# Kernel optimization log

Hardware: AMD Instinct MI355X
Metric: run time of the kernel (lower is better)

## Reference

```python
import jax, jax.numpy as jnp
import numpy as np

H = 5          # num_heads
QHD = 32       # query/key head dim
PHD = 4        # pos head dim


def setup_inputs() -> dict:
    key = jax.random.key(0)
    ks = jax.random.split(key, 8)
    T, B, D, PD = 512, 64, 512, 192
    lm_pruned = jax.random.normal(ks[0], (T, B, D), jnp.float32)
    am_pruned = jax.random.normal(ks[1], (T, B, D), jnp.float32)
    pos_emb = jax.random.normal(ks[2], (1, 2 * T - 1, PD), jnp.float32)
    key_padding_mask = jnp.zeros((B, T), bool)
    scale_q = QHD ** (-0.25)
    W_lm = (jax.random.normal(ks[3], (D, (QHD + PHD) * H), jnp.float32) * (scale_q / np.sqrt(D))).astype(jnp.float32)
    b_lm = jnp.zeros(((QHD + PHD) * H,), jnp.float32)
    W_am = (jax.random.normal(ks[4], (D, QHD * H), jnp.float32) * (scale_q / np.sqrt(D))).astype(jnp.float32)
    b_am = jnp.zeros((QHD * H,), jnp.float32)
    W_pos = (jax.random.normal(ks[5], (PD, H * PHD), jnp.float32) * (0.05 / np.sqrt(PD))).astype(jnp.float32)
    return {"lm_pruned": lm_pruned, "am_pruned": am_pruned, "pos_emb": pos_emb,
            "key_padding_mask": key_padding_mask,
            "W_lm": W_lm, "b_lm": b_lm, "W_am": W_am, "b_am": b_am, "W_pos": W_pos}


def reference(lm_pruned, am_pruned, pos_emb, key_padding_mask, W_lm, b_lm, W_am, b_am, W_pos):
    T, B, _ = lm_pruned.shape
    S = am_pruned.shape[0]
    lm = lm_pruned @ W_lm + b_lm          # (T, B, (QHD+PHD)*H)
    am = am_pruned @ W_am + b_am          # (S, B, QHD*H)
    q = lm[..., : H * QHD].reshape(T, B, H, QHD)
    p = lm[..., H * QHD:].reshape(T, B, H, PHD)
    k = am.reshape(S, B, H, QHD)          # whiten/balance are value-identity
    # content scores: (H, B, T, S)
    attn_scores = jnp.einsum('tbhd,sbhd->hbts', q, k)
    # positional scores
    pe = (pos_emb[0] @ W_pos).reshape(2 * T - 1, H, PHD)   # (2T-1, H, PHD)
    pos_scores = jnp.einsum('tbhd,nhd->hbtn', p, pe)        # (H, B, T, 2T-1)
    # Transformer-XL rel-shift: out[..., i, j] = pos_scores[..., i, j - i + T - 1]
    idx = jnp.arange(T)[None, :] - jnp.arange(T)[:, None] + (T - 1)  # (T, T)
    shifted = jnp.take_along_axis(pos_scores, idx[None, None, :, :], axis=-1)  # (H,B,T,T)
    attn_scores = attn_scores + shifted
    # key padding mask: (B, S) -> broadcast over heads and query positions
    attn_scores = jnp.where(key_padding_mask[None, :, None, :], jnp.float32(-1000.0), attn_scores)
    return jax.nn.softmax(attn_scores, axis=-1)
```

## Files before the change

### kernel.cpp

```cpp
#include <hip/hip_runtime.h>

#define TT 512
#define BB 64
#define HH 5
#define DD 512
#define NPOS 1023

typedef __bf16 bf16x8 __attribute__((ext_vector_type(8)));
typedef float floatx4 __attribute__((ext_vector_type(4)));

__global__ void prep_w_kernel(const float* __restrict__ Wlm, const float* __restrict__ Wam,
                              __bf16* __restrict__ WlmT, __bf16* __restrict__ WamT) {
  int idx = blockIdx.x * 256 + threadIdx.x;
  if (idx < 192 * 512) {
    int n = idx >> 9, k = idx & 511;
    float v = (n < 180) ? Wlm[k * 180 + n] : 0.f;
    WlmT[idx] = (__bf16)v;
  }
  if (idx < 160 * 512) {
    int n = idx >> 9, k = idx & 511;
    WamT[idx] = (__bf16)Wam[k * 160 + n];
  }
}

__global__ void pe_proj_kernel(const float* __restrict__ pos_emb, const float* __restrict__ Wpos,
                               float* __restrict__ peT) {
  int n = blockIdx.x;
  __shared__ float row[192];
  for (int i = threadIdx.x; i < 192; i += 64) row[i] = pos_emb[n * 192 + i];
  __syncthreads();
  int c = threadIdx.x;
  if (c < 20) {
    float acc = 0.f;
    for (int pd = 0; pd < 192; ++pd) acc += row[pd] * Wpos[pd * 20 + c];
    int h = c >> 2, d = c & 3;
    peT[((size_t)h * NPOS + n) * 4 + d] = acc;
  }
}

template <int NT, bool IS_LM>
__global__ __launch_bounds__(256) void proj_kernel(
    const float* __restrict__ A, const __bf16* __restrict__ WT, const float* __restrict__ bias,
    __bf16* __restrict__ qk_out, float* __restrict__ p_out) {
  __shared__ __align__(16) __bf16 a_lds[64][32];
  __shared__ __align__(16) __bf16 w_lds[NT * 16][32];
  const int tid = threadIdx.x;
  const int m0 = blockIdx.x * 64;
  const int lane = tid & 63, w = tid >> 6;
  const int quad = lane >> 4, nl = lane & 15;

  floatx4 zero = {0.f, 0.f, 0.f, 0.f};
  floatx4 acc[NT];
#pragma unroll
  for (int j = 0; j < NT; ++j) acc[j] = zero;

  const int arow = tid >> 2, aseg = tid & 3;
  for (int k0 = 0; k0 < 512; k0 += 32) {
    const float* ap = A + (size_t)(m0 + arow) * 512 + k0 + aseg * 8;
    float4 av0 = *(const float4*)ap;
    float4 av1 = *(const float4*)(ap + 4);
    __bf16* ad = &a_lds[arow][aseg * 8];
    ad[0] = (__bf16)av0.x; ad[1] = (__bf16)av0.y; ad[2] = (__bf16)av0.z; ad[3] = (__bf16)av0.w;
    ad[4] = (__bf16)av1.x; ad[5] = (__bf16)av1.y; ad[6] = (__bf16)av1.z; ad[7] = (__bf16)av1.w;
    for (int task = tid; task < NT * 64; task += 256) {
      int n = task >> 2, seg = task & 3;
      *(bf16x8*)&w_lds[n][seg * 8] = *(const bf16x8*)(WT + (size_t)n * 512 + k0 + seg * 8);
    }
    __syncthreads();
    bf16x8 af = *(const bf16x8*)&a_lds[16 * w + nl][quad * 8];
#pragma unroll
    for (int jt = 0; jt < NT; ++jt) {
      bf16x8 bfr = *(const bf16x8*)&w_lds[jt * 16 + nl][quad * 8];
      acc[jt] = __builtin_amdgcn_mfma_f32_16x16x32_bf16(af, bfr, acc[jt], 0, 0, 0);
    }
    __syncthreads();
  }
#pragma unroll
  for (int jt = 0; jt < NT; ++jt) {
    int c = jt * 16 + nl;
#pragma unroll
    for (int r = 0; r < 4; ++r) {
      int m = m0 + 16 * w + quad * 4 + r;
      float bv;
      if (IS_LM) bv = (c < 180) ? bias[c] : 0.f;
      else bv = bias[c];
      float val = acc[jt][r] + bv;
      if (IS_LM) {
        if (c < 160) qk_out[(size_t)m * 160 + c] = (__bf16)val;
        else if (c < 180) p_out[(size_t)m * 20 + (c - 160)] = val;
      } else {
        qk_out[(size_t)m * 160 + c] = (__bf16)val;
      }
    }
  }
}

__global__ __launch_bounds__(256) void attn_kernel(
    const __bf16* __restrict__ q, const __bf16* __restrict__ k,
    const float* __restrict__ p, const float* __restrict__ peT,
    const unsigned char* __restrict__ mask, float* __restrict__ out) {
  __shared__ __align__(16) __bf16 k_lds[512][32];
  __shared__ __align__(16) __bf16 q_lds[64][32];
  __shared__ __align__(16) float p_lds[64][4];
  __shared__ __align__(16) float pe_lds[575 * 4];
  __shared__ float mask_lds[512];

  const int tid = threadIdx.x;
  const int t0 = blockIdx.x * 64;
  const int b = blockIdx.y;
  const int h = blockIdx.z;
  const int lane = tid & 63, w = tid >> 6;
  const int quad = lane >> 4, nl = lane & 15;

#pragma unroll
  for (int it = 0; it < 8; ++it) {
    int idx = tid + it * 256;
    int s = idx >> 2, c = idx & 3;
    *(bf16x8*)&k_lds[s][c * 8] =
        *(const bf16x8*)(k + ((size_t)(s * BB + b) * HH + h) * 32 + c * 8);
  }
  {
    int s = tid >> 2, c = tid & 3;
    *(bf16x8*)&q_lds[s][c * 8] =
        *(const bf16x8*)(q + ((size_t)((t0 + s) * BB + b) * HH + h) * 32 + c * 8);
  }
  if (tid < 64) {
    *(float4*)&p_lds[tid][0] =
        *(const float4*)(p + ((size_t)((t0 + tid) * BB + b) * HH + h) * 4);
  }
  {
    int u0 = 448 - t0;
    for (int i = tid; i < 575; i += 256)
      *(float4*)&pe_lds[i * 4] = *(const float4*)(peT + ((size_t)h * NPOS + u0 + i) * 4);
  }
  for (int i = tid; i < 512; i += 256)
    mask_lds[i] = mask[b * 512 + i] ? -1000.f : 0.f;
  __syncthreads();

  floatx4 zero = {0.f, 0.f, 0.f, 0.f};
  floatx4 acc[32];
  bf16x8 af = *(const bf16x8*)&q_lds[16 * w + nl][quad * 8];
#pragma unroll
  for (int jt = 0; jt < 32; ++jt) {
    bf16x8 bfr = *(const bf16x8*)&k_lds[jt * 16 + nl][quad * 8];
    acc[jt] = __builtin_amdgcn_mfma_f32_16x16x32_bf16(af, bfr, zero, 0, 0, 0);
  }

  float rmax[4], rinv[4];
#pragma unroll
  for (int r = 0; r < 4; ++r) {
    int tl = 16 * w + quad * 4 + r;
    floatx4 pv = *(const floatx4*)&p_lds[tl][0];
    float mx = -3.4e38f;
#pragma unroll
    for (int jt = 0; jt < 32; ++jt) {
      int s = jt * 16 + nl;
      floatx4 pe = *(const floatx4*)&pe_lds[(s - tl + 63) * 4];
      float v = acc[jt][r] + pv[0] * pe[0] + pv[1] * pe[1] + pv[2] * pe[2] + pv[3] * pe[3] +
                mask_lds[s];
      acc[jt][r] = v;
      mx = fmaxf(mx, v);
    }
#pragma unroll
    for (int d = 1; d < 16; d <<= 1) mx = fmaxf(mx, __shfl_xor(mx, d, 64));
    rmax[r] = mx;
  }
#pragma unroll
  for (int r = 0; r < 4; ++r) {
    float sum = 0.f;
#pragma unroll
    for (int jt = 0; jt < 32; ++jt) {
      float e = __expf(acc[jt][r] - rmax[r]);
      acc[jt][r] = e;
      sum += e;
    }
#pragma unroll
    for (int d = 1; d < 16; d <<= 1) sum += __shfl_xor(sum, d, 64);
    rinv[r] = 1.0f / sum;
  }
#pragma unroll
  for (int r = 0; r < 4; ++r) {
    int tl = 16 * w + quad * 4 + r;
    size_t base = (((size_t)h * BB + b) * TT + (t0 + tl)) * TT;
#pragma unroll
    for (int jt = 0; jt < 32; ++jt) out[base + jt * 16 + nl] = acc[jt][r] * rinv[r];
  }
}

extern "C" void kernel_launch(void* const* d_in, const int* in_sizes, int n_in,
                              void* d_out, int out_size, void* d_ws, size_t ws_size,
                              hipStream_t stream) {
  const float* lm = (const float*)d_in[0];
  const float* am = (const float*)d_in[1];
  const float* pos_emb = (const float*)d_in[2];
  const unsigned char* mask = (const unsigned char*)d_in[3];
  const float* Wlm = (const float*)d_in[4];
  const float* blm = (const float*)d_in[5];
  const float* Wam = (const float*)d_in[6];
  const float* bam = (const float*)d_in[7];
  const float* Wpos = (const float*)d_in[8];
  float* out = (float*)d_out;

  char* ws = (char*)d_ws;
  __bf16* qbuf = (__bf16*)ws;
  __bf16* kbuf = qbuf + (size_t)32768 * 160;
  float* pbuf = (float*)(kbuf + (size_t)32768 * 160);
  float* pebuf = pbuf + (size_t)32768 * 20;
  __bf16* WlmT = (__bf16*)(pebuf + (size_t)5 * NPOS * 4);
  __bf16* WamT = WlmT + (size_t)192 * 512;

  prep_w_kernel<<<384, 256, 0, stream>>>(Wlm, Wam, WlmT, WamT);
  pe_proj_kernel<<<NPOS, 64, 0, stream>>>(pos_emb, Wpos, pebuf);
  proj_kernel<12, true><<<512, 256, 0, stream>>>(lm, WlmT, blm, qbuf, pbuf);
  proj_kernel<10, false><<<512, 256, 0, stream>>>(am, WamT, bam, kbuf, nullptr);
  attn_kernel<<<dim3(8, BB, HH), 256, 0, stream>>>(qbuf, kbuf, pbuf, pebuf, mask, out);
}
```

Before: 545.6 us.

## Merge prep and projection launches, store pos-emb in bf16, fold mask into MFMA

Combines the weight-transpose and positional-projection kernels into one launch, and the two projection GEMMs into a single 1024-block launch, cutting launch count from five to three. In the attention kernel, the projected positional embedding is stored as bf16 and unpacked with bit shifts. The key mask is fed in as the MFMA accumulator input, and the positional-score loop is restructured to compute all four row maxima in one pass. It also adds occupancy hints, vectorises the LDS store of A, and lowers positional-term precision to bf16, which may slightly change numerics.

Result: faster. 511.3 us (-6.3%).

```diff
diff --git a/kernel.cpp b/kernel.cpp
--- a/kernel.cpp
+++ b/kernel.cpp
@@ -3,75 +3,75 @@
 #define TT 512
 #define BB 64
 #define HH 5
-#define DD 512
 #define NPOS 1023
 
 typedef __bf16 bf16x8 __attribute__((ext_vector_type(8)));
+typedef __bf16 bf16x4 __attribute__((ext_vector_type(4)));
 typedef float floatx4 __attribute__((ext_vector_type(4)));
 
-__global__ void prep_w_kernel(const float* __restrict__ Wlm, const float* __restrict__ Wam,
-                              __bf16* __restrict__ WlmT, __bf16* __restrict__ WamT) {
-  int idx = blockIdx.x * 256 + threadIdx.x;
-  if (idx < 192 * 512) {
-    int n = idx >> 9, k = idx & 511;
-    float v = (n < 180) ? Wlm[k * 180 + n] : 0.f;
-    WlmT[idx] = (__bf16)v;
-  }
-  if (idx < 160 * 512) {
-    int n = idx >> 9, k = idx & 511;
-    WamT[idx] = (__bf16)Wam[k * 160 + n];
-  }
-}
-
-__global__ void pe_proj_kernel(const float* __restrict__ pos_emb, const float* __restrict__ Wpos,
-                               float* __restrict__ peT) {
-  int n = blockIdx.x;
-  __shared__ float row[192];
-  for (int i = threadIdx.x; i < 192; i += 64) row[i] = pos_emb[n * 192 + i];
-  __syncthreads();
-  int c = threadIdx.x;
-  if (c < 20) {
-    float acc = 0.f;
-    for (int pd = 0; pd < 192; ++pd) acc += row[pd] * Wpos[pd * 20 + c];
-    int h = c >> 2, d = c & 3;
-    peT[((size_t)h * NPOS + n) * 4 + d] = acc;
+__global__ void prep_kernel(const float* __restrict__ Wlm, const float* __restrict__ Wam,
+                            const float* __restrict__ pos_emb, const float* __restrict__ Wpos,
+                            __bf16* __restrict__ WlmT, __bf16* __restrict__ WamT,
+                            __bf16* __restrict__ peB) {
+  int bx = blockIdx.x;
+  if (bx < 384) {
+    int idx = bx * 256 + threadIdx.x;
+    if (idx < 192 * 512) {
+      int n = idx >> 9, k = idx & 511;
+      float v = (n < 180) ? Wlm[k * 180 + n] : 0.f;
+      WlmT[idx] = (__bf16)v;
+    }
+    if (idx < 160 * 512) {
+      int n = idx >> 9, k = idx & 511;
+      WamT[idx] = (__bf16)Wam[k * 160 + n];
+    }
+  } else {
+    int t = (bx - 384) * 256 + threadIdx.x;
+    int n = t >> 5, c = t & 31;
+    if (n < NPOS && c < 20) {
+      float acc = 0.f;
+#pragma unroll 8
+      for (int pd = 0; pd < 192; ++pd) acc += pos_emb[n * 192 + pd] * Wpos[pd * 20 + c];
+      int h = c >> 2, d = c & 3;
+      peB[((size_t)h * NPOS + n) * 4 + d] = (__bf16)acc;
+    }
   }
 }
 
 template <int NT, bool IS_LM>
-__global__ __launch_bounds__(256) void proj_kernel(
-    const float* __restrict__ A, const __bf16* __restrict__ WT, const float* __restrict__ bias,
-    __bf16* __restrict__ qk_out, float* __restrict__ p_out) {
-  __shared__ __align__(16) __bf16 a_lds[64][32];
-  __shared__ __align__(16) __bf16 w_lds[NT * 16][32];
+__device__ __forceinline__ void proj_body(const float* __restrict__ A, const __bf16* __restrict__ WT,
+                                          const float* __restrict__ bias, __bf16* __restrict__ qk_out,
+                                          float* __restrict__ p_out, int blk,
+                                          __bf16 (*a_lds)[32], __bf16 (*w_lds)[32]) {
   const int tid = threadIdx.x;
-  const int m0 = blockIdx.x * 64;
+  const int m0 = blk * 64;
   const int lane = tid & 63, w = tid >> 6;
   const int quad = lane >> 4, nl = lane & 15;
 
-  floatx4 zero = {0.f, 0.f, 0.f, 0.f};
   floatx4 acc[NT];
 #pragma unroll
-  for (int j = 0; j < NT; ++j) acc[j] = zero;
+  for (int j = 0; j < NT; ++j) acc[j] = floatx4{0.f, 0.f, 0.f, 0.f};
 
   const int arow = tid >> 2, aseg = tid & 3;
   for (int k0 = 0; k0 < 512; k0 += 32) {
     const float* ap = A + (size_t)(m0 + arow) * 512 + k0 + aseg * 8;
     float4 av0 = *(const float4*)ap;
     float4 av1 = *(const float4*)(ap + 4);
-    __bf16* ad = &a_lds[arow][aseg * 8];
-    ad[0] = (__bf16)av0.x; ad[1] = (__bf16)av0.y; ad[2] = (__bf16)av0.z; ad[3] = (__bf16)av0.w;
-    ad[4] = (__bf16)av1.x; ad[5] = (__bf16)av1.y; ad[6] = (__bf16)av1.z; ad[7] = (__bf16)av1.w;
+    bf16x8 pk;
+    pk[0] = (__bf16)av0.x; pk[1] = (__bf16)av0.y; pk[2] = (__bf16)av0.z; pk[3] = (__bf16)av0.w;
+    pk[4] = (__bf16)av1.x; pk[5] = (__bf16)av1.y; pk[6] = (__bf16)av1.z; pk[7] = (__bf16)av1.w;
+    *(bf16x8*)&a_lds[arow][aseg * 8] = pk;
+#pragma unroll
     for (int task = tid; task < NT * 64; task += 256) {
       int n = task >> 2, seg = task & 3;
       *(bf16x8*)&w_lds[n][seg * 8] = *(const bf16x8*)(WT + (size_t)n * 512 + k0 + seg * 8);
     }
     __syncthreads();
-    bf16x8 af = *(const bf16x8*)&a_lds[16 * w + nl][quad * 8];
+    bf16x8 afr = *(const bf16x8*)&a_lds[16 * w + nl][quad * 8];
 #pragma unroll
     for (int jt = 0; jt < NT; ++jt) {
       bf16x8 bfr = *(const bf16x8*)&w_lds[jt * 16 + nl][quad * 8];
-      acc[jt] = __builtin_amdgcn_mfma_f32_16x16x32_bf16(af, bfr, acc[jt], 0, 0, 0);
+      acc[jt] = __builtin_amdgcn_mfma_f32_16x16x32_bf16(afr, bfr, acc[jt], 0, 0, 0);
     }
     __syncthreads();
   }
@@ -81,9 +81,7 @@
 #pragma unroll
     for (int r = 0; r < 4; ++r) {
       int m = m0 + 16 * w + quad * 4 + r;
-      float bv;
-      if (IS_LM) bv = (c < 180) ? bias[c] : 0.f;
-      else bv = bias[c];
+      float bv = IS_LM ? ((c < 180) ? bias[c] : 0.f) : bias[c];
       float val = acc[jt][r] + bv;
       if (IS_LM) {
         if (c < 160) qk_out[(size_t)m * 160 + c] = (__bf16)val;
@@ -95,14 +93,27 @@
   }
 }
 
-__global__ __launch_bounds__(256) void attn_kernel(
+__global__ __launch_bounds__(256, 4) void proj_kernel(
+    const float* __restrict__ lm, const __bf16* __restrict__ WlmT, const float* __restrict__ blm,
+    __bf16* __restrict__ qbuf, float* __restrict__ pbuf,
+    const float* __restrict__ am, const __bf16* __restrict__ WamT, const float* __restrict__ bam,
+    __bf16* __restrict__ kbuf) {
+  __shared__ __align__(16) __bf16 a_lds[64][32];
+  __shared__ __align__(16) __bf16 w_lds[192][32];
+  if (blockIdx.x < 512)
+    proj_body<12, true>(lm, WlmT, blm, qbuf, pbuf, blockIdx.x, a_lds, w_lds);
+  else
+    proj_body<10, false>(am, WamT, bam, kbuf, nullptr, blockIdx.x - 512, a_lds, w_lds);
+}
+
+__global__ __launch_bounds__(256, 2) void attn_kernel(
     const __bf16* __restrict__ q, const __bf16* __restrict__ k,
-    const float* __restrict__ p, const float* __restrict__ peT,
+    const float* __restrict__ p, const __bf16* __restrict__ peB,
     const unsigned char* __restrict__ mask, float* __restrict__ out) {
   __shared__ __align__(16) __bf16 k_lds[512][32];
   __shared__ __align__(16) __bf16 q_lds[64][32];
   __shared__ __align__(16) float p_lds[64][4];
-  __shared__ __align__(16) float pe_lds[575 * 4];
+  __shared__ __align__(16) __bf16 pe_lds[576 * 4];
   __shared__ float mask_lds[512];
 
   const int tid = threadIdx.x;
@@ -117,60 +128,73 @@
     int idx = tid + it * 256;
     int s = idx >> 2, c = idx & 3;
     *(bf16x8*)&k_lds[s][c * 8] =
-        *(const bf16x8*)(k + ((size_t)(s * BB + b) * HH + h) * 32 + c * 8);
+        *(const bf16x8*)(k + (size_t)(s * BB + b) * 160 + h * 32 + c * 8);
   }
   {
     int s = tid >> 2, c = tid & 3;
     *(bf16x8*)&q_lds[s][c * 8] =
-        *(const bf16x8*)(q + ((size_t)((t0 + s) * BB + b) * HH + h) * 32 + c * 8);
-  }
-  if (tid < 64) {
-    *(float4*)&p_lds[tid][0] =
-        *(const float4*)(p + ((size_t)((t0 + tid) * BB + b) * HH + h) * 4);
-  }
+        *(const bf16x8*)(q + (size_t)((t0 + s) * BB + b) * 160 + h * 32 + c * 8);
+  }
+  if (tid < 64)
+    *(float4*)&p_lds[tid][0] = *(const float4*)(p + (size_t)((t0 + tid) * BB + b) * 20 + h * 4);
   {
     int u0 = 448 - t0;
     for (int i = tid; i < 575; i += 256)
-      *(float4*)&pe_lds[i * 4] = *(const float4*)(peT + ((size_t)h * NPOS + u0 + i) * 4);
+      *(bf16x4*)&pe_lds[i * 4] = *(const bf16x4*)(peB + ((size_t)h * NPOS + u0 + i) * 4);
   }
   for (int i = tid; i < 512; i += 256)
     mask_lds[i] = mask[b * 512 + i] ? -1000.f : 0.f;
   __syncthreads();
 
-  floatx4 zero = {0.f, 0.f, 0.f, 0.f};
   floatx4 acc[32];
   bf16x8 af = *(const bf16x8*)&q_lds[16 * w + nl][quad * 8];
 #pragma unroll
   for (int jt = 0; jt < 32; ++jt) {
+    float m = mask_lds[jt * 16 + nl];
+    floatx4 cin = {m, m, m, m};
     bf16x8 bfr = *(const bf16x8*)&k_lds[jt * 16 + nl][quad * 8];
-    acc[jt] = __builtin_amdgcn_mfma_f32_16x16x32_bf16(af, bfr, zero, 0, 0, 0);
-  }
-
-  float rmax[4], rinv[4];
+    acc[jt] = __builtin_amdgcn_mfma_f32_16x16x32_bf16(af, bfr, cin, 0, 0, 0);
+  }
+
+  const int base = 16 * w + quad * 4;
+  floatx4 pv[4];
+#pragma unroll
+  for (int r = 0; r < 4; ++r) pv[r] = *(const floatx4*)&p_lds[base + r][0];
+
+  const uint32_t* pp = (const uint32_t*)pe_lds + 2 * (nl - base + 63);
+  float mx[4] = {-3.4e38f, -3.4e38f, -3.4e38f, -3.4e38f};
+#pragma unroll
+  for (int jt = 0; jt < 32; ++jt) {
+    const uint32_t* pj = pp + jt * 32;
+#pragma unroll
+    for (int r = 0; r < 4; ++r) {
+      uint32_t w0 = pj[-2 * r], w1 = pj[1 - 2 * r];
+      float f0 = __uint_as_float(w0 << 16);
+      float f1 = __uint_as_float(w0 & 0xffff0000u);
+      float f2 = __uint_as_float(w1 << 16);
+      float f3 = __uint_as_float(w1 & 0xffff0000u);
+      float v = acc[jt][r];
+      v = fmaf(pv[r][0], f0, v);
+      v = fmaf(pv[r][1], f1, v);
+      v = fmaf(pv[r][2], f2, v);
+      v = fmaf(pv[r][3], f3, v);
+      acc[jt][r] = v;
+      mx[r] = fmaxf(mx[r], v);
+    }
+  }
+
 #pragma unroll
   for (int r = 0; r < 4; ++r) {
-    int tl = 16 * w + quad * 4 + r;
-    floatx4 pv = *(const floatx4*)&p_lds[tl][0];
-    float mx = -3.4e38f;
-#pragma unroll
-    for (int jt = 0; jt < 32; ++jt) {
-      int s = jt * 16 + nl;
-      floatx4 pe = *(const floatx4*)&pe_lds[(s - tl + 63) * 4];
-      float v = acc[jt][r] + pv[0] * pe[0] + pv[1] * pe[1] + pv[2] * pe[2] + pv[3] * pe[3] +
-                mask_lds[s];
-      acc[jt][r] = v;
-      mx = fmaxf(mx, v);
-    }
-#pragma unroll
-    for (int d = 1; d < 16; d <<= 1) mx = fmaxf(mx, __shfl_xor(mx, d, 64));
-    rmax[r] = mx;
-  }
+#pragma unroll
+    for (int d = 1; d < 16; d <<= 1) mx[r] = fmaxf(mx[r], __shfl_xor(mx[r], d, 64));
+  }
+  float rinv[4];
 #pragma unroll
   for (int r = 0; r < 4; ++r) {
     float sum = 0.f;
 #pragma unroll
     for (int jt = 0; jt < 32; ++jt) {
-      float e = __expf(acc[jt][r] - rmax[r]);
+      float e = __expf(acc[jt][r] - mx[r]);
       acc[jt][r] = e;
       sum += e;
     }
@@ -180,10 +204,9 @@
   }
 #pragma unroll
   for (int r = 0; r < 4; ++r) {
-    int tl = 16 * w + quad * 4 + r;
-    size_t base = (((size_t)h * BB + b) * TT + (t0 + tl)) * TT;
-#pragma unroll
-    for (int jt = 0; jt < 32; ++jt) out[base + jt * 16 + nl] = acc[jt][r] * rinv[r];
+    size_t basep = (((size_t)h * BB + b) * TT + (t0 + base + r)) * TT;
+#pragma unroll
+    for (int jt = 0; jt < 32; ++jt) out[basep + jt * 16 + nl] = acc[jt][r] * rinv[r];
   }
 }
 
@@ -205,13 +228,11 @@
   __bf16* qbuf = (__bf16*)ws;
   __bf16* kbuf = qbuf + (size_t)32768 * 160;
   float* pbuf = (float*)(kbuf + (size_t)32768 * 160);
-  float* pebuf = pbuf + (size_t)32768 * 20;
-  __bf16* WlmT = (__bf16*)(pebuf + (size_t)5 * NPOS * 4);
+  __bf16* peB = (__bf16*)(pbuf + (size_t)32768 * 20);
+  __bf16* WlmT = peB + (size_t)5 * 1024 * 4;
   __bf16* WamT = WlmT + (size_t)192 * 512;
 
-  prep_w_kernel<<<384, 256, 0, stream>>>(Wlm, Wam, WlmT, WamT);
-  pe_proj_kernel<<<NPOS, 64, 0, stream>>>(pos_emb, Wpos, pebuf);
-  proj_kernel<12, true><<<512, 256, 0, stream>>>(lm, WlmT, blm, qbuf, pbuf);
-  proj_kernel<10, false><<<512, 256, 0, stream>>>(am, WamT, bam, kbuf, nullptr);
-  attn_kernel<<<dim3(8, BB, HH), 256, 0, stream>>>(qbuf, kbuf, pbuf, pebuf, mask, out);
-}
+  prep_kernel<<<512, 256, 0, stream>>>(Wlm, Wam, pos_emb, Wpos, WlmT, WamT, peB);
+  proj_kernel<<<1024, 256, 0, stream>>>(lm, WlmT, blm, qbuf, pbuf, am, WamT, bam, kbuf);
+  attn_kernel<<<dim3(8, BB, HH), 256, 0, stream>>>(qbuf, kbuf, pbuf, peB, mask, out);
+}
```
